# Performance work log

Measured on AMD Instinct MI355X. Metric: run time of the kernel, lower is better.

The kernel has to match this reference:

```python
import jax, jax.numpy as jnp
import numpy as np

B, T, N, D = 16, 48, 256, 64
K_HEADS = 8


def setup_inputs() -> dict:
    key = jax.random.key(0)
    ks = jax.random.split(key, 12)
    return {
        "query": jax.random.normal(ks[0], (B, T, N, D), jnp.float32),
        "key": jax.random.normal(ks[1], (B, T, N, D), jnp.float32),
        "value": jax.random.normal(ks[2], (B, T, N, D), jnp.float32),
        "key_w": jax.random.normal(ks[3], (B, T, D, D), jnp.float32) * 0.05,
        "key_b": jax.random.normal(ks[4], (B, T, D), jnp.float32) * 0.05,
        "value_w": jax.random.normal(ks[5], (B, T, D, D), jnp.float32) * 0.05,
        "value_b": jax.random.normal(ks[6], (B, T, D), jnp.float32) * 0.05,
        "proj1_w": jax.random.normal(ks[7], (D, D), jnp.float32) * 0.05,
        "proj1_b": jax.random.normal(ks[8], (D,), jnp.float32) * 0.05,
        "proj2_w": jax.random.normal(ks[9], (D, D), jnp.float32) * 0.05,
        "proj2_b": jax.random.normal(ks[10], (D,), jnp.float32) * 0.05,
        "rate": jnp.full((1,), 0.8, jnp.float32),
    }


def reference(query, key, value, key_w, key_b, value_w, value_b,
              proj1_w, proj1_b, proj2_w, proj2_b, rate):
    b, t, n, d = query.shape
    hs = d // K_HEADS
    # per-(batch,time) projections (LinearCustom)
    k = jnp.einsum('btnd,btde->btne', key, key_w) + key_b[:, :, None, :]
    v = jnp.einsum('btnd,btde->btne', value, value_w) + value_b[:, :, None, :]
    # split heads along channel dim (matches torch.split on dim -1)
    qh = query.reshape(b, t, n, K_HEADS, hs)
    kh = k.reshape(b, t, n, K_HEADS, hs)
    vh = v.reshape(b, t, n, K_HEADS, hs)
    # scores: [b, h, n, q, k]
    scores = jnp.einsum('bqnhd,bknhd->bhnqk', qh, kh) / jnp.sqrt(jnp.asarray(hs, query.dtype))
    # time decay: b_time_decays[..., i, j] = (T-1-i) + 1 = T - i (depends on query pos only)
    dec = (t - jnp.arange(t, dtype=scores.dtype))[:, None]  # [T, 1], broadcasts over key axis
    s = jax.nn.sigmoid(scores)
    denom = 1.0 + jax.nn.sigmoid(s * jax.nn.sigmoid(rate) * dec)
    att = jax.nn.softmax(jnp.tanh(s / denom), axis=-1)
    x = jnp.einsum('bhnqk,bknhd->bqnhd', att, vh).reshape(b, t, n, d)
    x = jnp.tanh(x @ proj1_w.T + proj1_b)
    return x @ proj2_w.T + proj2_b
```

## Files before the change

### kernel.cpp

```cpp
#include <hip/hip_runtime.h>


#define B_ 16
#define T_ 48
#define N_ 256
#define D_ 64

__device__ __forceinline__ float rcpf(float x) { return __builtin_amdgcn_rcpf(x); }
__device__ __forceinline__ float ex2(float x) { return __builtin_amdgcn_exp2f(x); }
#define LOG2E 1.4426950408889634f

__global__ __launch_bounds__(256) void proj_kv_kernel(
    const float* __restrict__ key, const float* __restrict__ key_w, const float* __restrict__ key_b,
    const float* __restrict__ value, const float* __restrict__ value_w, const float* __restrict__ value_b,
    float* __restrict__ k_out, float* __restrict__ v_out)
{
    const int bt = blockIdx.x;
    const int which = blockIdx.y;
    const float* __restrict__ in = (which ? value : key) + (size_t)bt * N_ * D_;
    const float* __restrict__ w  = (which ? value_w : key_w) + (size_t)bt * D_ * D_;
    const float* __restrict__ bb = (which ? value_b : key_b) + (size_t)bt * D_;
    float* __restrict__ out = (which ? v_out : k_out) + (size_t)bt * N_ * D_;

    __shared__ float Wl[D_][D_];
    __shared__ float Xl[128][68];
    __shared__ float Bl[D_];

    const int tid = threadIdx.x;
    #pragma unroll
    for (int i = tid; i < D_ * D_; i += 256) Wl[i >> 6][i & 63] = w[i];
    if (tid < D_) Bl[tid] = bb[tid];

    const int cg = tid & 7;
    const int rg = tid >> 3;

    for (int n0 = 0; n0 < N_; n0 += 128) {
        __syncthreads();
        #pragma unroll
        for (int i = tid; i < 128 * D_ / 4; i += 256) {
            const int e = i * 4;
            *(float4*)&Xl[e >> 6][e & 63] = *(const float4*)&in[(size_t)n0 * D_ + e];
        }
        __syncthreads();

        float acc[4][8];
        #pragma unroll
        for (int j = 0; j < 4; ++j)
            #pragma unroll
            for (int i = 0; i < 8; ++i) acc[j][i] = Bl[cg * 8 + i];

        #pragma unroll 8
        for (int d = 0; d < D_; ++d) {
            const float4 w0 = *(const float4*)&Wl[d][cg * 8];
            const float4 w1 = *(const float4*)&Wl[d][cg * 8 + 4];
            #pragma unroll
            for (int j = 0; j < 4; ++j) {
                const float a = Xl[rg + 32 * j][d];
                acc[j][0] += a * w0.x; acc[j][1] += a * w0.y;
                acc[j][2] += a * w0.z; acc[j][3] += a * w0.w;
                acc[j][4] += a * w1.x; acc[j][5] += a * w1.y;
                acc[j][6] += a * w1.z; acc[j][7] += a * w1.w;
            }
        }

        #pragma unroll
        for (int j = 0; j < 4; ++j) {
            const size_t row = (size_t)(n0 + rg + 32 * j);
            *(float4*)&out[row * D_ + cg * 8]     = make_float4(acc[j][0], acc[j][1], acc[j][2], acc[j][3]);
            *(float4*)&out[row * D_ + cg * 8 + 4] = make_float4(acc[j][4], acc[j][5], acc[j][6], acc[j][7]);
        }
    }
}

__global__ __launch_bounds__(256) void attn_kernel(
    const float* __restrict__ query, float* __restrict__ k_xatt, const float* __restrict__ v_in,
    const float* __restrict__ rate)
{
    const int b  = blockIdx.x >> 7;
    const int n0 = (blockIdx.x & 127) * 2;

    __shared__ float K[2][T_][68];
    __shared__ float V[2][T_][68];

    const int tid = threadIdx.x;
    #pragma unroll
    for (int i = tid; i < T_ * 16; i += 256) {
        const int t = i >> 4, d4 = (i & 15) * 4;
        const size_t g0 = ((size_t)(b * T_ + t) * N_ + n0) * D_ + d4;
        *(float4*)&K[0][t][d4] = *(const float4*)&k_xatt[g0];
        *(float4*)&V[0][t][d4] = *(const float4*)&v_in[g0];
        *(float4*)&K[1][t][d4] = *(const float4*)&k_xatt[g0 + D_];
        *(float4*)&V[1][t][d4] = *(const float4*)&v_in[g0 + D_];
    }
    const float rsig = rcpf(1.0f + ex2(-rate[0] * LOG2E));

    const int nl = tid >> 7;
    const int r  = tid & 127;
    const int qg = r >> 3;
    const int h  = r & 7;
    const int n  = n0 + nl;

    const float C1 = 0.35355339059327373f * LOG2E;
    float4 qa[3], qb[3];
    float rdn[3];
    #pragma unroll
    for (int j = 0; j < 3; ++j) {
        const int q = qg + 16 * j;
        const size_t g = ((size_t)(b * T_ + q) * N_ + n) * D_ + h * 8;
        const float4 a = *(const float4*)&query[g];
        const float4 c = *(const float4*)&query[g + 4];
        qa[j] = make_float4(-C1 * a.x, -C1 * a.y, -C1 * a.z, -C1 * a.w);
        qb[j] = make_float4(-C1 * c.x, -C1 * c.y, -C1 * c.z, -C1 * c.w);
        rdn[j] = -rsig * (float)(T_ - q) * LOG2E;
    }
    __syncthreads();

    float4 acc0[3], acc1[3];
    float ssum[3];
    #pragma unroll
    for (int j = 0; j < 3; ++j) {
        acc0[j] = make_float4(0.f, 0.f, 0.f, 0.f);
        acc1[j] = make_float4(0.f, 0.f, 0.f, 0.f);
        ssum[j] = 0.f;
    }

    #pragma unroll 4
    for (int tk = 0; tk < T_; ++tk) {
        const float4 ka = *(const float4*)&K[nl][tk][h * 8];
        const float4 kb = *(const float4*)&K[nl][tk][h * 8 + 4];
        const float4 va = *(const float4*)&V[nl][tk][h * 8];
        const float4 vb = *(const float4*)&V[nl][tk][h * 8 + 4];
        #pragma unroll
        for (int j = 0; j < 3; ++j) {
            const float dn = qa[j].x * ka.x + qa[j].y * ka.y + qa[j].z * ka.z + qa[j].w * ka.w
                           + qb[j].x * kb.x + qb[j].y * kb.y + qb[j].z * kb.z + qb[j].w * kb.w;
            const float E1  = ex2(dn);
            const float s   = rcpf(1.0f + E1);
            const float E2  = ex2(s * rdn[j]);
            const float arg = s * (1.0f + E2) * rcpf(2.0f + E2);
            const float x2  = arg * arg;
            const float th  = arg * (15.0f + x2) * rcpf(15.0f + 6.0f * x2);
            const float e   = ex2(th * LOG2E);
            ssum[j] += e;
            acc0[j].x += e * va.x; acc0[j].y += e * va.y; acc0[j].z += e * va.z; acc0[j].w += e * va.w;
            acc1[j].x += e * vb.x; acc1[j].y += e * vb.y; acc1[j].z += e * vb.z; acc1[j].w += e * vb.w;
        }
    }

    #pragma unroll
    for (int j = 0; j < 3; ++j) {
        const float inv = rcpf(ssum[j]);
        const int q = qg + 16 * j;
        const size_t g = ((size_t)(b * T_ + q) * N_ + n) * D_ + h * 8;
        *(float4*)&k_xatt[g]     = make_float4(acc0[j].x * inv, acc0[j].y * inv, acc0[j].z * inv, acc0[j].w * inv);
        *(float4*)&k_xatt[g + 4] = make_float4(acc1[j].x * inv, acc1[j].y * inv, acc1[j].z * inv, acc1[j].w * inv);
    }
}

__global__ __launch_bounds__(256) void wtrans_kernel(
    const float* __restrict__ p1w, const float* __restrict__ p2w,
    float* __restrict__ w1t, float* __restrict__ w2t)
{
    const int i = blockIdx.x * 256 + threadIdx.x;
    if (i < D_ * D_) {
        const int d = i >> 6, c = i & 63;
        w1t[i] = p1w[c * 64 + d];
        w2t[i] = p2w[c * 64 + d];
    }
}

__global__ __launch_bounds__(256) void out_proj_kernel(
    const float* __restrict__ xatt,
    const float* __restrict__ w1t, const float* __restrict__ p1b,
    const float* __restrict__ w2t, const float* __restrict__ p2b,
    float* __restrict__ out)
{
    __shared__ float X[128][68];

    const int tid = threadIdx.x;
    const size_t m0 = (size_t)blockIdx.x * 128;

    #pragma unroll
    for (int i = tid; i < 128 * 16; i += 256) {
        const int row = i >> 4, d4 = (i & 15) * 4;
        *(float4*)&X[row][d4] = *(const float4*)&xatt[(m0 + row) * D_ + d4];
    }
    __syncthreads();

    const int cg = tid & 7;
    const int rg = tid >> 3;

    float x1[4][8];
    {
        float acc[4][8];
        #pragma unroll
        for (int i = 0; i < 8; ++i) {
            const float bv = p1b[cg * 8 + i];
            #pragma unroll
            for (int j = 0; j < 4; ++j) acc[j][i] = bv;
        }
        #pragma unroll 2
        for (int d0 = 0; d0 < D_; d0 += 4) {
            float4 w0[4], w1[4];
            #pragma unroll
            for (int dd = 0; dd < 4; ++dd) {
                w0[dd] = *(const float4*)&w1t[(d0 + dd) * 64 + cg * 8];
                w1[dd] = *(const float4*)&w1t[(d0 + dd) * 64 + cg * 8 + 4];
            }
            #pragma unroll
            for (int j = 0; j < 4; ++j) {
                const float4 xv = *(const float4*)&X[rg + 32 * j][d0];
                acc[j][0] += xv.x * w0[0].x + xv.y * w0[1].x + xv.z * w0[2].x + xv.w * w0[3].x;
                acc[j][1] += xv.x * w0[0].y + xv.y * w0[1].y + xv.z * w0[2].y + xv.w * w0[3].y;
                acc[j][2] += xv.x * w0[0].z + xv.y * w0[1].z + xv.z * w0[2].z + xv.w * w0[3].z;
                acc[j][3] += xv.x * w0[0].w + xv.y * w0[1].w + xv.z * w0[2].w + xv.w * w0[3].w;
                acc[j][4] += xv.x * w1[0].x + xv.y * w1[1].x + xv.z * w1[2].x + xv.w * w1[3].x;
                acc[j][5] += xv.x * w1[0].y + xv.y * w1[1].y + xv.z * w1[2].y + xv.w * w1[3].y;
                acc[j][6] += xv.x * w1[0].z + xv.y * w1[1].z + xv.z * w1[2].z + xv.w * w1[3].z;
                acc[j][7] += xv.x * w1[0].w + xv.y * w1[1].w + xv.z * w1[2].w + xv.w * w1[3].w;
            }
        }
        #pragma unroll
        for (int j = 0; j < 4; ++j)
            #pragma unroll
            for (int i = 0; i < 8; ++i)
                x1[j][i] = 1.0f - 2.0f * rcpf(ex2(acc[j][i] * (2.0f * LOG2E)) + 1.0f);
    }
    __syncthreads();
    #pragma unroll
    for (int j = 0; j < 4; ++j) {
        *(float4*)&X[rg + 32 * j][cg * 8]     = make_float4(x1[j][0], x1[j][1], x1[j][2], x1[j][3]);
        *(float4*)&X[rg + 32 * j][cg * 8 + 4] = make_float4(x1[j][4], x1[j][5], x1[j][6], x1[j][7]);
    }
    __syncthreads();

    {
        float acc[4][8];
        #pragma unroll
        for (int i = 0; i < 8; ++i) {
            const float bv = p2b[cg * 8 + i];
            #pragma unroll
            for (int j = 0; j < 4; ++j) acc[j][i] = bv;
        }
        #pragma unroll 2
        for (int d0 = 0; d0 < D_; d0 += 4) {
            float4 w0[4], w1[4];
            #pragma unroll
            for (int dd = 0; dd < 4; ++dd) {
                w0[dd] = *(const float4*)&w2t[(d0 + dd) * 64 + cg * 8];
                w1[dd] = *(const float4*)&w2t[(d0 + dd) * 64 + cg * 8 + 4];
            }
            #pragma unroll
            for (int j = 0; j < 4; ++j) {
                const float4 xv = *(const float4*)&X[rg + 32 * j][d0];
                acc[j][0] += xv.x * w0[0].x + xv.y * w0[1].x + xv.z * w0[2].x + xv.w * w0[3].x;
                acc[j][1] += xv.x * w0[0].y + xv.y * w0[1].y + xv.z * w0[2].y + xv.w * w0[3].y;
                acc[j][2] += xv.x * w0[0].z + xv.y * w0[1].z + xv.z * w0[2].z + xv.w * w0[3].z;
                acc[j][3] += xv.x * w0[0].w + xv.y * w0[1].w + xv.z * w0[2].w + xv.w * w0[3].w;
                acc[j][4] += xv.x * w1[0].x + xv.y * w1[1].x + xv.z * w1[2].x + xv.w * w1[3].x;
                acc[j][5] += xv.x * w1[0].y + xv.y * w1[1].y + xv.z * w1[2].y + xv.w * w1[3].y;
                acc[j][6] += xv.x * w1[0].z + xv.y * w1[1].z + xv.z * w1[2].z + xv.w * w1[3].z;
                acc[j][7] += xv.x * w1[0].w + xv.y * w1[1].w + xv.z * w1[2].w + xv.w * w1[3].w;
            }
        }
        #pragma unroll
        for (int j = 0; j < 4; ++j) {
            const size_t og = (m0 + rg + 32 * j) * D_ + cg * 8;
            *(float4*)&out[og]     = make_float4(acc[j][0], acc[j][1], acc[j][2], acc[j][3]);
            *(float4*)&out[og + 4] = make_float4(acc[j][4], acc[j][5], acc[j][6], acc[j][7]);
        }
    }
}

extern "C" void kernel_launch(void* const* d_in, const int* in_sizes, int n_in,
                              void* d_out, int out_size, void* d_ws, size_t ws_size,
                              hipStream_t stream) {
    const float* query   = (const float*)d_in[0];
    const float* key     = (const float*)d_in[1];
    const float* value   = (const float*)d_in[2];
    const float* key_w   = (const float*)d_in[3];
    const float* key_b   = (const float*)d_in[4];
    const float* value_w = (const float*)d_in[5];
    const float* value_b = (const float*)d_in[6];
    const float* p1w     = (const float*)d_in[7];
    const float* p1b     = (const float*)d_in[8];
    const float* p2w     = (const float*)d_in[9];
    const float* p2b     = (const float*)d_in[10];
    const float* rate    = (const float*)d_in[11];
    float* out = (float*)d_out;

    float* kws = (float*)d_ws;
    float* vws = kws + (size_t)B_ * T_ * N_ * D_;
    float* w1t = vws;
    float* w2t = vws + D_ * D_;

    dim3 gridA(B_ * T_, 2);
    proj_kv_kernel<<<gridA, 256, 0, stream>>>(key, key_w, key_b, value, value_w, value_b, kws, vws);
    attn_kernel<<<B_ * (N_ / 2), 256, 0, stream>>>(query, kws, vws, rate);
    wtrans_kernel<<<16, 256, 0, stream>>>(p1w, p2w, w1t, w2t);
    out_proj_kernel<<<(B_ * T_ * N_) / 128, 256, 0, stream>>>(kws, w1t, p1b, w2t, p2b, out);
}
```

Measured before the change: 237.9 us.

## Use 8x8 register tiles with 128-thread blocks and LDS-staged weights in projection GEMMs

Both projection kernels move from 4x8 to 8x8 per-thread output tiles with 128-thread blocks, and share one GEMM macro that reads 4-wide d chunks as float4. proj_kv now splits the N dimension across a third grid axis instead of looping over it inside the block. out_proj stages each weight matrix in LDS rather than reading it from global memory. The aim is more FMAs per LDS load and fewer global weight reads, at the cost of higher register pressure and fewer threads per block.

```diff
diff --git a/kernel.cpp b/kernel.cpp
--- a/kernel.cpp
+++ b/kernel.cpp
@@ -10,65 +10,78 @@
 __device__ __forceinline__ float ex2(float x) { return __builtin_amdgcn_exp2f(x); }
 #define LOG2E 1.4426950408889634f
 
-__global__ __launch_bounds__(256) void proj_kv_kernel(
+#define GEMM8x8_D4(acc, XLDS, WLDS, d0, rowg, colg)                              \
+    {                                                                            \
+        float4 xv[8], w0[4], w1[4];                                              \
+        _Pragma("unroll")                                                        \
+        for (int dd = 0; dd < 4; ++dd) {                                         \
+            w0[dd] = *(const float4*)&WLDS[d0 + dd][colg * 8];                   \
+            w1[dd] = *(const float4*)&WLDS[d0 + dd][colg * 8 + 4];               \
+        }                                                                        \
+        _Pragma("unroll")                                                        \
+        for (int j = 0; j < 8; ++j) xv[j] = *(const float4*)&XLDS[rowg + 16 * j][d0]; \
+        _Pragma("unroll")                                                        \
+        for (int j = 0; j < 8; ++j) {                                            \
+            acc[j][0] += xv[j].x * w0[0].x + xv[j].y * w0[1].x + xv[j].z * w0[2].x + xv[j].w * w0[3].x; \
+            acc[j][1] += xv[j].x * w0[0].y + xv[j].y * w0[1].y + xv[j].z * w0[2].y + xv[j].w * w0[3].y; \
+            acc[j][2] += xv[j].x * w0[0].z + xv[j].y * w0[1].z + xv[j].z * w0[2].z + xv[j].w * w0[3].z; \
+            acc[j][3] += xv[j].x * w0[0].w + xv[j].y * w0[1].w + xv[j].z * w0[2].w + xv[j].w * w0[3].w; \
+            acc[j][4] += xv[j].x * w1[0].x + xv[j].y * w1[1].x + xv[j].z * w1[2].x + xv[j].w * w1[3].x; \
+            acc[j][5] += xv[j].x * w1[0].y + xv[j].y * w1[1].y + xv[j].z * w1[2].y + xv[j].w * w1[3].y; \
+            acc[j][6] += xv[j].x * w1[0].z + xv[j].y * w1[1].z + xv[j].z * w1[2].z + xv[j].w * w1[3].z; \
+            acc[j][7] += xv[j].x * w1[0].w + xv[j].y * w1[1].w + xv[j].z * w1[2].w + xv[j].w * w1[3].w; \
+        }                                                                        \
+    }
+
+__global__ __launch_bounds__(128) void proj_kv_kernel(
     const float* __restrict__ key, const float* __restrict__ key_w, const float* __restrict__ key_b,
     const float* __restrict__ value, const float* __restrict__ value_w, const float* __restrict__ value_b,
     float* __restrict__ k_out, float* __restrict__ v_out)
 {
     const int bt = blockIdx.x;
     const int which = blockIdx.y;
-    const float* __restrict__ in = (which ? value : key) + (size_t)bt * N_ * D_;
+    const int n0 = blockIdx.z * 128;
+    const float* __restrict__ in = (which ? value : key) + ((size_t)bt * N_ + n0) * D_;
     const float* __restrict__ w  = (which ? value_w : key_w) + (size_t)bt * D_ * D_;
     const float* __restrict__ bb = (which ? value_b : key_b) + (size_t)bt * D_;
-    float* __restrict__ out = (which ? v_out : k_out) + (size_t)bt * N_ * D_;
-
+    float* __restrict__ out = (which ? v_out : k_out) + ((size_t)bt * N_ + n0) * D_;
+
+    __shared__ float Xl[128][68];
     __shared__ float Wl[D_][D_];
-    __shared__ float Xl[128][68];
     __shared__ float Bl[D_];
 
     const int tid = threadIdx.x;
     #pragma unroll
-    for (int i = tid; i < D_ * D_; i += 256) Wl[i >> 6][i & 63] = w[i];
+    for (int i = tid; i < D_ * D_ / 4; i += 128)
+        ((float4*)&Wl[0][0])[i] = ((const float4*)w)[i];
     if (tid < D_) Bl[tid] = bb[tid];
-
-    const int cg = tid & 7;
-    const int rg = tid >> 3;
-
-    for (int n0 = 0; n0 < N_; n0 += 128) {
-        __syncthreads();
-        #pragma unroll
-        for (int i = tid; i < 128 * D_ / 4; i += 256) {
-            const int e = i * 4;
-            *(float4*)&Xl[e >> 6][e & 63] = *(const float4*)&in[(size_t)n0 * D_ + e];
-        }
-        __syncthreads();
-
-        float acc[4][8];
-        #pragma unroll
-        for (int j = 0; j < 4; ++j)
-            #pragma unroll
-            for (int i = 0; i < 8; ++i) acc[j][i] = Bl[cg * 8 + i];
-
-        #pragma unroll 8
-        for (int d = 0; d < D_; ++d) {
-            const float4 w0 = *(const float4*)&Wl[d][cg * 8];
-            const float4 w1 = *(const float4*)&Wl[d][cg * 8 + 4];
-            #pragma unroll
-            for (int j = 0; j < 4; ++j) {
-                const float a = Xl[rg + 32 * j][d];
-                acc[j][0] += a * w0.x; acc[j][1] += a * w0.y;
-                acc[j][2] += a * w0.z; acc[j][3] += a * w0.w;
-                acc[j][4] += a * w1.x; acc[j][5] += a * w1.y;
-                acc[j][6] += a * w1.z; acc[j][7] += a * w1.w;
-            }
-        }
-
-        #pragma unroll
-        for (int j = 0; j < 4; ++j) {
-            const size_t row = (size_t)(n0 + rg + 32 * j);
-            *(float4*)&out[row * D_ + cg * 8]     = make_float4(acc[j][0], acc[j][1], acc[j][2], acc[j][3]);
-            *(float4*)&out[row * D_ + cg * 8 + 4] = make_float4(acc[j][4], acc[j][5], acc[j][6], acc[j][7]);
-        }
+    #pragma unroll
+    for (int i = tid; i < 128 * 16; i += 128) {
+        const int row = i >> 4, d4 = (i & 15) * 4;
+        *(float4*)&Xl[row][d4] = *(const float4*)&in[i * 4];
+    }
+    __syncthreads();
+
+    const int colg = tid & 7;
+    const int rowg = tid >> 3;
+
+    float acc[8][8];
+    #pragma unroll
+    for (int i = 0; i < 8; ++i) {
+        const float bv = Bl[colg * 8 + i];
+        #pragma unroll
+        for (int j = 0; j < 8; ++j) acc[j][i] = bv;
+    }
+
+    #pragma unroll 2
+    for (int d0 = 0; d0 < D_; d0 += 4)
+        GEMM8x8_D4(acc, Xl, Wl, d0, rowg, colg)
+
+    #pragma unroll
+    for (int j = 0; j < 8; ++j) {
+        const size_t og = (size_t)(rowg + 16 * j) * D_ + colg * 8;
+        *(float4*)&out[og]     = make_float4(acc[j][0], acc[j][1], acc[j][2], acc[j][3]);
+        *(float4*)&out[og + 4] = make_float4(acc[j][4], acc[j][5], acc[j][6], acc[j][7]);
     }
 }
 
@@ -169,103 +182,75 @@
     }
 }
 
-__global__ __launch_bounds__(256) void out_proj_kernel(
+__global__ __launch_bounds__(128) void out_proj_kernel(
     const float* __restrict__ xatt,
     const float* __restrict__ w1t, const float* __restrict__ p1b,
     const float* __restrict__ w2t, const float* __restrict__ p2b,
     float* __restrict__ out)
 {
     __shared__ float X[128][68];
+    __shared__ float Wl[D_][D_];
 
     const int tid = threadIdx.x;
     const size_t m0 = (size_t)blockIdx.x * 128;
 
     #pragma unroll
-    for (int i = tid; i < 128 * 16; i += 256) {
+    for (int i = tid; i < D_ * D_ / 4; i += 128)
+        ((float4*)&Wl[0][0])[i] = ((const float4*)w1t)[i];
+    #pragma unroll
+    for (int i = tid; i < 128 * 16; i += 128) {
         const int row = i >> 4, d4 = (i & 15) * 4;
         *(float4*)&X[row][d4] = *(const float4*)&xatt[(m0 + row) * D_ + d4];
     }
     __syncthreads();
 
-    const int cg = tid & 7;
-    const int rg = tid >> 3;
-
-    float x1[4][8];
+    const int colg = tid & 7;
+    const int rowg = tid >> 3;
+
+    float x1[8][8];
     {
-        float acc[4][8];
+        float acc[8][8];
         #pragma unroll
         for (int i = 0; i < 8; ++i) {
-            const float bv = p1b[cg * 8 + i];
+            const float bv = p1b[colg * 8 + i];
             #pragma unroll
-            for (int j = 0; j < 4; ++j) acc[j][i] = bv;
+            for (int j = 0; j < 8; ++j) acc[j][i] = bv;
         }
         #pragma unroll 2
-        for (int d0 = 0; d0 < D_; d0 += 4) {
-            float4 w0[4], w1[4];
-            #pragma unroll
-            for (int dd = 0; dd < 4; ++dd) {
-                w0[dd] = *(const float4*)&w1t[(d0 + dd) * 64 + cg * 8];
-                w1[dd] = *(const float4*)&w1t[(d0 + dd) * 64 + cg * 8 + 4];
-            }
-            #pragma unroll
-            for (int j = 0; j < 4; ++j) {
-                const float4 xv = *(const float4*)&X[rg + 32 * j][d0];
-                acc[j][0] += xv.x * w0[0].x + xv.y * w0[1].x + xv.z * w0[2].x + xv.w * w0[3].x;
-                acc[j][1] += xv.x * w0[0].y + xv.y * w0[1].y + xv.z * w0[2].y + xv.w * w0[3].y;
-                acc[j][2] += xv.x * w0[0].z + xv.y * w0[1].z + xv.z * w0[2].z + xv.w * w0[3].z;
-                acc[j][3] += xv.x * w0[0].w + xv.y * w0[1].w + xv.z * w0[2].w + xv.w * w0[3].w;
-                acc[j][4] += xv.x * w1[0].x + xv.y * w1[1].x + xv.z * w1[2].x + xv.w * w1[3].x;
-                acc[j][5] += xv.x * w1[0].y + xv.y * w1[1].y + xv.z * w1[2].y + xv.w * w1[3].y;
-                acc[j][6] += xv.x * w1[0].z + xv.y * w1[1].z + xv.z * w1[2].z + xv.w * w1[3].z;
-                acc[j][7] += xv.x * w1[0].w + xv.y * w1[1].w + xv.z * w1[2].w + xv.w * w1[3].w;
-            }
-        }
-        #pragma unroll
-        for (int j = 0; j < 4; ++j)
+        for (int d0 = 0; d0 < D_; d0 += 4)
+            GEMM8x8_D4(acc, X, Wl, d0, rowg, colg)
+        #pragma unroll
+        for (int j = 0; j < 8; ++j)
             #pragma unroll
             for (int i = 0; i < 8; ++i)
                 x1[j][i] = 1.0f - 2.0f * rcpf(ex2(acc[j][i] * (2.0f * LOG2E)) + 1.0f);
     }
     __syncthreads();
-    #pragma unroll
-    for (int j = 0; j < 4; ++j) {
-        *(float4*)&X[rg + 32 * j][cg * 8]     = make_float4(x1[j][0], x1[j][1], x1[j][2], x1[j][3]);
-        *(float4*)&X[rg + 32 * j][cg * 8 + 4] = make_float4(x1[j][4], x1[j][5], x1[j][6], x1[j][7]);
-    }
+
+    #pragma unroll
+    for (int j = 0; j < 8; ++j) {
+        *(float4*)&X[rowg + 16 * j][colg * 8]     = make_float4(x1[j][0], x1[j][1], x1[j][2], x1[j][3]);
+        *(float4*)&X[rowg + 16 * j][colg * 8 + 4] = make_float4(x1[j][4], x1[j][5], x1[j][6], x1[j][7]);
+    }
+    #pragma unroll
+    for (int i = tid; i < D_ * D_ / 4; i += 128)
+        ((float4*)&Wl[0][0])[i] = ((const float4*)w2t)[i];
     __syncthreads();
 
     {
-        float acc[4][8];
+        float acc[8][8];
         #pragma unroll
         for (int i = 0; i < 8; ++i) {
-            const float bv = p2b[cg * 8 + i];
+            const float bv = p2b[colg * 8 + i];
             #pragma unroll
-            for (int j = 0; j < 4; ++j) acc[j][i] = bv;
+            for (int j = 0; j < 8; ++j) acc[j][i] = bv;
         }
         #pragma unroll 2
-        for (int d0 = 0; d0 < D_; d0 += 4) {
-            float4 w0[4], w1[4];
-            #pragma unroll
-            for (int dd = 0; dd < 4; ++dd) {
-                w0[dd] = *(const float4*)&w2t[(d0 + dd) * 64 + cg * 8];
-                w1[dd] = *(const float4*)&w2t[(d0 + dd) * 64 + cg * 8 + 4];
-            }
-            #pragma unroll
-            for (int j = 0; j < 4; ++j) {
-                const float4 xv = *(const float4*)&X[rg + 32 * j][d0];
-                acc[j][0] += xv.x * w0[0].x + xv.y * w0[1].x + xv.z * w0[2].x + xv.w * w0[3].x;
-                acc[j][1] += xv.x * w0[0].y + xv.y * w0[1].y + xv.z * w0[2].y + xv.w * w0[3].y;
-                acc[j][2] += xv.x * w0[0].z + xv.y * w0[1].z + xv.z * w0[2].z + xv.w * w0[3].z;
-                acc[j][3] += xv.x * w0[0].w + xv.y * w0[1].w + xv.z * w0[2].w + xv.w * w0[3].w;
-                acc[j][4] += xv.x * w1[0].x + xv.y * w1[1].x + xv.z * w1[2].x + xv.w * w1[3].x;
-                acc[j][5] += xv.x * w1[0].y + xv.y * w1[1].y + xv.z * w1[2].y + xv.w * w1[3].y;
-                acc[j][6] += xv.x * w1[0].z + xv.y * w1[1].z + xv.z * w1[2].z + xv.w * w1[3].z;
-                acc[j][7] += xv.x * w1[0].w + xv.y * w1[1].w + xv.z * w1[2].w + xv.w * w1[3].w;
-            }
-        }
-        #pragma unroll
-        for (int j = 0; j < 4; ++j) {
-            const size_t og = (m0 + rg + 32 * j) * D_ + cg * 8;
+        for (int d0 = 0; d0 < D_; d0 += 4)
+            GEMM8x8_D4(acc, X, Wl, d0, rowg, colg)
+        #pragma unroll
+        for (int j = 0; j < 8; ++j) {
+            const size_t og = (m0 + rowg + 16 * j) * D_ + colg * 8;
             *(float4*)&out[og]     = make_float4(acc[j][0], acc[j][1], acc[j][2], acc[j][3]);
             *(float4*)&out[og + 4] = make_float4(acc[j][4], acc[j][5], acc[j][6], acc[j][7]);
         }
@@ -294,9 +279,9 @@
     float* w1t = vws;
     float* w2t = vws + D_ * D_;
 
-    dim3 gridA(B_ * T_, 2);
-    proj_kv_kernel<<<gridA, 256, 0, stream>>>(key, key_w, key_b, value, value_w, value_b, kws, vws);
+    dim3 gridA(B_ * T_, 2, 2);
+    proj_kv_kernel<<<gridA, 128, 0, stream>>>(key, key_w, key_b, value, value_w, value_b, kws, vws);
     attn_kernel<<<B_ * (N_ / 2), 256, 0, stream>>>(query, kws, vws, rate);
     wtrans_kernel<<<16, 256, 0, stream>>>(p1w, p2w, w1t, w2t);
-    out_proj_kernel<<<(B_ * T_ * N_) / 128, 256, 0, stream>>>(kws, w1t, p1b, w2t, p2b, out);
-}
+    out_proj_kernel<<<(B_ * T_ * N_) / 128, 128, 0, stream>>>(kws, w1t, p1b, w2t, p2b, out);
+}
```

After: 258.1 us. +8.5%, slower.
